# Performance work log

Measured on AMD Instinct MI355X. Metric: run time of the kernel, lower is better.

The kernel has to match this reference:

```python
import jax, jax.numpy as jnp
import numpy as np

DIM = 1024
H = 16
HD = DIM // H
EPS = 1e-5


def setup_inputs() -> dict:
    key = jax.random.key(0)
    ks = jax.random.split(key, 12)
    B, S = 4, 2048
    s = 0.02
    return {
        "q": jax.random.normal(ks[0], (B, S, DIM), jnp.float32),
        "k": jax.random.normal(ks[1], (B, S, DIM), jnp.float32),
        "v": jax.random.normal(ks[2], (B, S, DIM), jnp.float32),
        "Wq": jax.random.normal(ks[3], (DIM, DIM), jnp.float32) * s,
        "bq": jnp.zeros((DIM,), jnp.float32),
        "Wk": jax.random.normal(ks[4], (DIM, DIM), jnp.float32) * s,
        "bk": jnp.zeros((DIM,), jnp.float32),
        "Wv": jax.random.normal(ks[5], (DIM, DIM), jnp.float32) * s,
        "bv": jnp.zeros((DIM,), jnp.float32),
        "Wo": jax.random.normal(ks[6], (DIM, DIM), jnp.float32) * s,
        "bo": jnp.zeros((DIM,), jnp.float32),
        "gamma": jnp.ones((DIM,), jnp.float32),
        "beta": jnp.zeros((DIM,), jnp.float32),
    }


def reference(q, k, v, Wq, bq, Wk, bk, Wv, bv, Wo, bo, gamma, beta):
    B, S, _ = q.shape
    scale = HD ** -0.5
    # projections -> [B, H, S, HD]
    def proj(x, W, b):
        return (x @ W.T + b).reshape(B, -1, H, HD).transpose(0, 2, 1, 3)
    qh = proj(q, Wq, bq)
    kh = proj(k, Wk, bk)
    vh = proj(v, Wv, bv)
    scores = jnp.einsum("bhsd,bhtd->bhst", qh, kh) * scale  # [B,H,S,S]
    attn = jax.nn.softmax(scores, axis=-1)  # dropout is identity in eval
    out = jnp.einsum("bhst,bhtd->bhsd", attn, vh)
    out = out.transpose(0, 2, 1, 3).reshape(B, S, DIM)
    out = out @ Wo.T + bo
    # LayerNorm
    mu = out.mean(-1, keepdims=True)
    var = out.var(-1, keepdims=True)
    return (out - mu) * jax.lax.rsqrt(var + EPS) * gamma + beta
```

## Files before the change

kernel.cpp:

```cpp
#include <hip/hip_runtime.h>

typedef unsigned short u16;
typedef __attribute__((ext_vector_type(8))) short bf16x8;
typedef __attribute__((ext_vector_type(4))) float f32x4;
typedef __attribute__((ext_vector_type(16))) float f32x16;
typedef __attribute__((ext_vector_type(4))) unsigned short u16x4;
typedef __attribute__((ext_vector_type(4))) unsigned int u32x4;
typedef __attribute__((ext_vector_type(2))) unsigned int u32x2;

#define DIM 1024
#define NH 16
#define HD 64
#define BATCH 4
#define SEQ 2048
#define MROWS (BATCH * SEQ)

__device__ __forceinline__ u16 f2bf(float f) {
  unsigned u = __builtin_bit_cast(unsigned, f);
  return (u16)((u + 0x7fffu + ((u >> 16) & 1u)) >> 16);
}

__device__ __forceinline__ void gload16(const u16* g, u16* l) {
  __builtin_amdgcn_global_load_lds(
      (const __attribute__((address_space(1))) void*)g,
      (__attribute__((address_space(3))) void*)l, 16, 0, 0);
}

__device__ __forceinline__ unsigned cvtpk(float lo, float hi) {
  unsigned r;
  asm("v_cvt_pk_bf16_f32 %0, %1, %2" : "=v"(r) : "v"(lo), "v"(hi));
  return r;
}

__device__ __forceinline__ void plswap(unsigned& a, unsigned& b) {
  asm("v_permlane32_swap_b32 %0, %1" : "+v"(a), "+v"(b));
}

__global__ __launch_bounds__(256) void cvtw_kernel(const float* __restrict__ Wq,
                                                   const float* __restrict__ Wk,
                                                   const float* __restrict__ Wv,
                                                   const float* __restrict__ Wo,
                                                   u16* __restrict__ dst,
                                                   float scale) {
  int i = blockIdx.x * blockDim.x + threadIdx.x;
  int seg = i >> 18;
  int off = i & ((1 << 18) - 1);
  const float* src = (seg == 0) ? Wq : (seg == 1) ? Wk : (seg == 2) ? Wv : Wo;
  float mul = (seg == 0) ? scale : 1.f;
  f32x4 v = ((const f32x4*)src)[off];
  u16x4 o;
  o[0] = f2bf(v[0] * mul);
  o[1] = f2bf(v[1] * mul);
  o[2] = f2bf(v[2] * mul);
  o[3] = f2bf(v[3] * mul);
  ((u16x4*)dst)[i] = o;
}

enum { EPI_QK = 0, EPI_VT = 1, EPI_F32 = 2 };

#define BM 128
#define BN 128
#define BK 64

template <int EPI, bool AF32, bool BF32>
__global__ __launch_bounds__(256) void gemm_nt(const void* __restrict__ Ap,
                                               const void* __restrict__ Bp,
                                               void* __restrict__ C,
                                               const float* __restrict__ bias,
                                               float bscale, int Kdim) {
  __shared__ __attribute__((aligned(16))) u16 Alds[BM * BK];
  __shared__ __attribute__((aligned(16))) u16 Blds[BN * BK];

  const int tid = threadIdx.x;
  const int w = tid >> 6, l = tid & 63;
  const int wr = w >> 1, wc = w & 1;
  const int row0 = blockIdx.y * BM;
  const int col0 = blockIdx.x * BN;
  const int lr = l >> 3;
  const int sp = l & 7;

  f32x4 acc[4][4];
#pragma unroll
  for (int i = 0; i < 4; i++)
#pragma unroll
    for (int j = 0; j < 4; j++) {
      f32x4 z = {0.f, 0.f, 0.f, 0.f};
      acc[i][j] = z;
    }

  for (int k0 = 0; k0 < Kdim; k0 += BK) {
    __syncthreads();
#pragma unroll
    for (int q = 0; q < 4; q++) {
      int chunk = w * 4 + q;
      int r = chunk * 8 + lr;
      int sl = sp ^ (r & 7);
      if constexpr (AF32) {
        const float* s = (const float*)Ap + (size_t)(row0 + r) * Kdim + k0 + sp * 8;
        f32x4 v0 = *(const f32x4*)s;
        f32x4 v1 = *(const f32x4*)(s + 4);
        u32x4 pk;
        pk[0] = cvtpk(v0[0], v0[1]);
        pk[1] = cvtpk(v0[2], v0[3]);
        pk[2] = cvtpk(v1[0], v1[1]);
        pk[3] = cvtpk(v1[2], v1[3]);
        *(u32x4*)&Alds[r * 64 + sl * 8] = pk;
      } else {
        gload16((const u16*)Ap + (size_t)(row0 + r) * Kdim + k0 + sl * 8,
                &Alds[chunk * 512]);
      }
      if constexpr (BF32) {
        const float* s = (const float*)Bp + (size_t)(col0 + r) * Kdim + k0 + sp * 8;
        f32x4 v0 = *(const f32x4*)s;
        f32x4 v1 = *(const f32x4*)(s + 4);
        u32x4 pk;
        pk[0] = cvtpk(v0[0], v0[1]);
        pk[1] = cvtpk(v0[2], v0[3]);
        pk[2] = cvtpk(v1[0], v1[1]);
        pk[3] = cvtpk(v1[2], v1[3]);
        *(u32x4*)&Blds[r * 64 + sl * 8] = pk;
      } else {
        gload16((const u16*)Bp + (size_t)(col0 + r) * Kdim + k0 + sl * 8,
                &Blds[chunk * 512]);
      }
    }
    __syncthreads();

#pragma unroll
    for (int t = 0; t < 2; t++) {
      int slot = (t * 4 + (l >> 4)) ^ (l & 7);
      bf16x8 af[4], bf[4];
#pragma unroll
      for (int i = 0; i < 4; i++) {
        int arow = wr * 64 + i * 16 + (l & 15);
        af[i] = *(const bf16x8*)&Alds[arow * 64 + slot * 8];
        int brow = wc * 64 + i * 16 + (l & 15);
        bf[i] = *(const bf16x8*)&Blds[brow * 64 + slot * 8];
      }
      __builtin_amdgcn_s_setprio(1);
#pragma unroll
      for (int i = 0; i < 4; i++)
#pragma unroll
        for (int j = 0; j < 4; j++)
          acc[i][j] = __builtin_amdgcn_mfma_f32_16x16x32_bf16(af[i], bf[j],
                                                              acc[i][j], 0, 0, 0);
      __builtin_amdgcn_s_setprio(0);
    }
  }

#pragma unroll
  for (int i = 0; i < 4; i++) {
#pragma unroll
    for (int j = 0; j < 4; j++) {
#pragma unroll
      for (int q = 0; q < 4; q++) {
        int m = row0 + wr * 64 + i * 16 + (l >> 4) * 4 + q;
        int n = col0 + wc * 64 + j * 16 + (l & 15);
        float v = acc[i][j][q];
        if (EPI == EPI_QK) {
          v += bias[n] * bscale;
          int b_ = m >> 11, s_ = m & (SEQ - 1), h_ = n >> 6, hd_ = n & 63;
          ((u16*)C)[(((size_t)(b_ * NH + h_) * SEQ + s_) << 6) + hd_] = f2bf(v);
        } else if (EPI == EPI_VT) {
          v += bias[m];
          int b_ = n >> 11, s_ = n & (SEQ - 1);
          ((u16*)C)[((size_t)(b_ * NH + (m >> 6)) * HD + (m & 63)) * SEQ + s_] =
              f2bf(v);
        } else {
          v += bias[n];
          ((float*)C)[(size_t)m * DIM + n] = v;
        }
      }
    }
  }
}

__global__ __launch_bounds__(256, 2) void attn_kernel(const u16* __restrict__ Qh,
                                                      const u16* __restrict__ Kh,
                                                      const u16* __restrict__ Vt,
                                                      u16* __restrict__ AO) {
  __shared__ __attribute__((aligned(16))) u16 Klds[3][64 * 64];
  __shared__ __attribute__((aligned(16))) u16 Vlds[3][64 * 64];

  const int tid = threadIdx.x;
  const int w = tid >> 6, l = tid & 63;
  const int l31 = l & 31, hi = l >> 5;
  const int p = blockIdx.x;
  const int bh = (p & 7) + 8 * (p >> 6);
  const int qt = (p >> 3) & 7;
  const int b_ = bh >> 4, h_ = bh & 15;
  const int lr = l >> 3, sp = l & 7;

  const int qrowA = qt * 256 + w * 64 + l31;
  const int qrowB = qrowA + 32;
  const u16* qpA = Qh + ((size_t)bh * SEQ + qrowA) * HD + hi * 8;
  const u16* qpB = Qh + ((size_t)bh * SEQ + qrowB) * HD + hi * 8;
  bf16x8 qfA[4], qfB[4];
#pragma unroll
  for (int ks = 0; ks < 4; ks++) {
    qfA[ks] = *(const bf16x8*)(qpA + ks * 16);
    qfB[ks] = *(const bf16x8*)(qpB + ks * 16);
  }

  f32x16 oA0, oA1, oB0, oB1;
#pragma unroll
  for (int r = 0; r < 16; r++) {
    oA0[r] = 0.f;
    oA1[r] = 0.f;
    oB0[r] = 0.f;
    oB1[r] = 0.f;
  }
  float lrunA = 0.f, lrunB = 0.f;

  const int chunk = w * 2;
  const int r0 = chunk * 8 + lr, r1 = r0 + 8;
  const int sl0 = sp ^ (lr & 7);
  const size_t kbase = (size_t)bh * SEQ * HD;
  const size_t vbase = (size_t)bh * HD * SEQ;

#define ISSUE(kt, buf)                                                        \
  do {                                                                        \
    gload16(Kh + kbase + ((kt) * 64 + r0) * HD + sl0 * 8,                     \
            &Klds[buf][chunk * 512]);                                         \
    gload16(Vt + vbase + (size_t)r0 * SEQ + (kt) * 64 + sl0 * 8,              \
            &Vlds[buf][chunk * 512]);                                         \
    gload16(Kh + kbase + ((kt) * 64 + r1) * HD + sl0 * 8,                     \
            &Klds[buf][chunk * 512 + 512]);                                   \
    gload16(Vt + vbase + (size_t)r1 * SEQ + (kt) * 64 + sl0 * 8,              \
            &Vlds[buf][chunk * 512 + 512]);                                   \
  } while (0)

  ISSUE(0, 0);

  int cur = 0;
  for (int kt = 0; kt < SEQ / 64; kt++) {
    const int nxt = (cur == 2) ? 0 : cur + 1;
    if (kt < SEQ / 64 - 1) {
      ISSUE(kt + 1, nxt);
      asm volatile("s_waitcnt vmcnt(4)" ::: "memory");
    } else {
      asm volatile("s_waitcnt vmcnt(0)" ::: "memory");
    }
    __builtin_amdgcn_s_barrier();
    __builtin_amdgcn_sched_barrier(0);

    const u16* Kc = Klds[cur];
    const u16* Vc = Vlds[cur];

    f32x16 sA0, sA1, sB0, sB1;
#pragma unroll
    for (int r = 0; r < 16; r++) {
      sA0[r] = 0.f;
      sA1[r] = 0.f;
      sB0[r] = 0.f;
      sB1[r] = 0.f;
    }
    __builtin_amdgcn_s_setprio(1);
#pragma unroll
    for (int ks = 0; ks < 4; ks++) {
      int slot = ((ks * 2 + hi) ^ (l & 7)) * 8;
      bf16x8 kf0 = *(const bf16x8*)&Kc[l31 * 64 + slot];
      bf16x8 kf1 = *(const bf16x8*)&Kc[(32 + l31) * 64 + slot];
      sA0 = __builtin_amdgcn_mfma_f32_32x32x16_bf16(kf0, qfA[ks], sA0, 0, 0, 0);
      sA1 = __builtin_amdgcn_mfma_f32_32x32x16_bf16(kf1, qfA[ks], sA1, 0, 0, 0);
      sB0 = __builtin_amdgcn_mfma_f32_32x32x16_bf16(kf0, qfB[ks], sB0, 0, 0, 0);
      sB1 = __builtin_amdgcn_mfma_f32_32x32x16_bf16(kf1, qfB[ks], sB1, 0, 0, 0);
    }
    __builtin_amdgcn_s_setprio(0);

#pragma unroll
    for (int r = 0; r < 16; r++) {
      sA0[r] = __builtin_amdgcn_exp2f(sA0[r]);
      sA1[r] = __builtin_amdgcn_exp2f(sA1[r]);
      sB0[r] = __builtin_amdgcn_exp2f(sB0[r]);
      sB1[r] = __builtin_amdgcn_exp2f(sB1[r]);
    }
    float ta[16], tb[16];
#pragma unroll
    for (int r = 0; r < 8; r++) {
      ta[r] = sA0[2 * r] + sA0[2 * r + 1];
      ta[8 + r] = sA1[2 * r] + sA1[2 * r + 1];
      tb[r] = sB0[2 * r] + sB0[2 * r + 1];
      tb[8 + r] = sB1[2 * r] + sB1[2 * r + 1];
    }
#pragma unroll
    for (int s2 = 8; s2 > 0; s2 >>= 1)
#pragma unroll
      for (int r = 0; r < 8; r++)
        if (r < s2) {
          ta[r] += ta[r + s2];
          tb[r] += tb[r + s2];
        }
    float psA = ta[0];
    float psB = tb[0];
    psA += __shfl_xor(psA, 32);
    psB += __shfl_xor(psB, 32);
    lrunA += psA;
    lrunB += psB;

    unsigned cwA[2][4][2], cwB[2][4][2];
#pragma unroll
    for (int g = 0; g < 4; g++) {
      cwA[0][g][0] = cvtpk(sA0[4 * g], sA0[4 * g + 1]);
      cwA[0][g][1] = cvtpk(sA0[4 * g + 2], sA0[4 * g + 3]);
      cwA[1][g][0] = cvtpk(sA1[4 * g], sA1[4 * g + 1]);
      cwA[1][g][1] = cvtpk(sA1[4 * g + 2], sA1[4 * g + 3]);
      cwB[0][g][0] = cvtpk(sB0[4 * g], sB0[4 * g + 1]);
      cwB[0][g][1] = cvtpk(sB0[4 * g + 2], sB0[4 * g + 3]);
      cwB[1][g][0] = cvtpk(sB1[4 * g], sB1[4 * g + 1]);
      cwB[1][g][1] = cvtpk(sB1[4 * g + 2], sB1[4 * g + 3]);
    }
    bf16x8 paA[4], paB[4];
#pragma unroll
    for (int ks = 0; ks < 4; ks++) {
      int t = ks >> 1, c = ks & 1;
      {
        unsigned a0 = cwA[t][2 * c][0], b0 = cwA[t][2 * c + 1][0];
        unsigned a1 = cwA[t][2 * c][1], b1 = cwA[t][2 * c + 1][1];
        plswap(a0, b0);
        plswap(a1, b1);
        u32x4 pw;
        pw[0] = a0;
        pw[1] = a1;
        pw[2] = b0;
        pw[3] = b1;
        paA[ks] = __builtin_bit_cast(bf16x8, pw);
      }
      {
        unsigned a0 = cwB[t][2 * c][0], b0 = cwB[t][2 * c + 1][0];
        unsigned a1 = cwB[t][2 * c][1], b1 = cwB[t][2 * c + 1][1];
        plswap(a0, b0);
        plswap(a1, b1);
        u32x4 pw;
        pw[0] = a0;
        pw[1] = a1;
        pw[2] = b0;
        pw[3] = b1;
        paB[ks] = __builtin_bit_cast(bf16x8, pw);
      }
    }

    __builtin_amdgcn_s_setprio(1);
#pragma unroll
    for (int ks = 0; ks < 4; ks++) {
      int slot = ((ks * 2 + hi) ^ (l & 7)) * 8;
      bf16x8 vf0 = *(const bf16x8*)&Vc[l31 * 64 + slot];
      bf16x8 vf1 = *(const bf16x8*)&Vc[(32 + l31) * 64 + slot];
      oA0 = __builtin_amdgcn_mfma_f32_32x32x16_bf16(vf0, paA[ks], oA0, 0, 0, 0);
      oA1 = __builtin_amdgcn_mfma_f32_32x32x16_bf16(vf1, paA[ks], oA1, 0, 0, 0);
      oB0 = __builtin_amdgcn_mfma_f32_32x32x16_bf16(vf0, paB[ks], oB0, 0, 0, 0);
      oB1 = __builtin_amdgcn_mfma_f32_32x32x16_bf16(vf1, paB[ks], oB1, 0, 0, 0);
    }
    __builtin_amdgcn_s_setprio(0);

    cur = nxt;
  }

  float rinvA = 1.f / lrunA;
  float rinvB = 1.f / lrunB;
  u16* orowA = AO + ((size_t)b_ * SEQ + qrowA) * DIM + h_ * HD;
  u16* orowB = AO + ((size_t)b_ * SEQ + qrowB) * DIM + h_ * HD;
#pragma unroll
  for (int g = 0; g < 4; g++) {
    u32x2 s0, s1;
    s0[0] = cvtpk(oA0[4 * g] * rinvA, oA0[4 * g + 1] * rinvA);
    s0[1] = cvtpk(oA0[4 * g + 2] * rinvA, oA0[4 * g + 3] * rinvA);
    s1[0] = cvtpk(oA1[4 * g] * rinvA, oA1[4 * g + 1] * rinvA);
    s1[1] = cvtpk(oA1[4 * g + 2] * rinvA, oA1[4 * g + 3] * rinvA);
    *(u32x2*)(orowA + 8 * g + 4 * hi) = s0;
    *(u32x2*)(orowA + 32 + 8 * g + 4 * hi) = s1;
    s0[0] = cvtpk(oB0[4 * g] * rinvB, oB0[4 * g + 1] * rinvB);
    s0[1] = cvtpk(oB0[4 * g + 2] * rinvB, oB0[4 * g + 3] * rinvB);
    s1[0] = cvtpk(oB1[4 * g] * rinvB, oB1[4 * g + 1] * rinvB);
    s1[1] = cvtpk(oB1[4 * g + 2] * rinvB, oB1[4 * g + 3] * rinvB);
    *(u32x2*)(orowB + 8 * g + 4 * hi) = s0;
    *(u32x2*)(orowB + 32 + 8 * g + 4 * hi) = s1;
  }
}

__global__ __launch_bounds__(256) void ln_kernel(const float* __restrict__ X,
                                                 const float* __restrict__ gamma,
                                                 const float* __restrict__ beta,
                                                 float* __restrict__ out) {
  __shared__ float red[8];
  const int row = blockIdx.x;
  const int tid = threadIdx.x;
  const float* xr = X + (size_t)row * DIM;
  f32x4 v = ((const f32x4*)xr)[tid];
  float s = v[0] + v[1] + v[2] + v[3];
  float ss = v[0] * v[0] + v[1] * v[1] + v[2] * v[2] + v[3] * v[3];
#pragma unroll
  for (int mm = 1; mm <= 32; mm <<= 1) {
    s += __shfl_xor(s, mm);
    ss += __shfl_xor(ss, mm);
  }
  const int w = tid >> 6, l = tid & 63;
  if (l == 0) {
    red[w * 2] = s;
    red[w * 2 + 1] = ss;
  }
  __syncthreads();
  s = red[0] + red[2] + red[4] + red[6];
  ss = red[1] + red[3] + red[5] + red[7];
  float mu = s * (1.f / DIM);
  float var = ss * (1.f / DIM) - mu * mu;
  float rstd = rsqrtf(var + 1e-5f);
  f32x4 g = ((const f32x4*)gamma)[tid];
  f32x4 bt = ((const f32x4*)beta)[tid];
  f32x4 o;
#pragma unroll
  for (int j = 0; j < 4; j++) o[j] = (v[j] - mu) * rstd * g[j] + bt[j];
  ((f32x4*)(out + (size_t)row * DIM))[tid] = o;
}

extern "C" void kernel_launch(void* const* d_in, const int* in_sizes, int n_in,
                              void* d_out, int out_size, void* d_ws,
                              size_t ws_size, hipStream_t stream) {
  (void)in_sizes; (void)n_in; (void)out_size; (void)ws_size;
  const float* q = (const float*)d_in[0];
  const float* k = (const float*)d_in[1];
  const float* v = (const float*)d_in[2];
  const float* Wq = (const float*)d_in[3];
  const float* bq = (const float*)d_in[4];
  const float* Wk = (const float*)d_in[5];
  const float* bk = (const float*)d_in[6];
  const float* Wv = (const float*)d_in[7];
  const float* bv = (const float*)d_in[8];
  const float* Wo = (const float*)d_in[9];
  const float* bo = (const float*)d_in[10];
  const float* gamma = (const float*)d_in[11];
  const float* beta = (const float*)d_in[12];

  char* ws = (char*)d_ws;
  const size_t MiB = 1 << 20;
  u16* Wb = (u16*)(ws + 0 * MiB);
  u16* Wq_b = Wb;
  u16* Wk_b = (u16*)(ws + 2 * MiB);
  u16* Wv_b = (u16*)(ws + 4 * MiB);
  u16* Wo_b = (u16*)(ws + 6 * MiB);
  u16* Qh = (u16*)(ws + 8 * MiB);
  u16* Kh = (u16*)(ws + 24 * MiB);
  u16* Vt = (u16*)(ws + 40 * MiB);
  u16* AO = (u16*)(ws + 56 * MiB);

  const float scale = 0.125f * 1.44269504088896f;

  cvtw_kernel<<<4096, 256, 0, stream>>>(Wq, Wk, Wv, Wo, Wb, scale);

  dim3 blk(256);
  gemm_nt<EPI_QK, true, false><<<dim3(DIM / BN, MROWS / BM), blk, 0, stream>>>(
      q, Wq_b, Qh, bq, scale, DIM);
  gemm_nt<EPI_QK, true, false><<<dim3(DIM / BN, MROWS / BM), blk, 0, stream>>>(
      k, Wk_b, Kh, bk, 1.f, DIM);
  gemm_nt<EPI_VT, false, true><<<dim3(MROWS / BN, DIM / BM), blk, 0, stream>>>(
      Wv_b, v, Vt, bv, 1.f, DIM);

  attn_kernel<<<512, 256, 0, stream>>>(Qh, Kh, Vt, AO);

  gemm_nt<EPI_F32, false, false><<<dim3(DIM / BN, MROWS / BM), blk, 0, stream>>>(
      AO, Wo_b, (float*)d_out, bo, 1.f, DIM);

  ln_kernel<<<MROWS, 256, 0, stream>>>((const float*)d_out, gamma, beta,
                                       (float*)d_out);
}
```

Baseline: 238.6 us.

## Double-buffer LDS tiles in GEMM to overlap next-tile loads with MFMA

```diff
diff --git a/kernel.cpp b/kernel.cpp
--- a/kernel.cpp
+++ b/kernel.cpp
@@ -68,8 +68,8 @@
                                                void* __restrict__ C,
                                                const float* __restrict__ bias,
                                                float bscale, int Kdim) {
-  __shared__ __attribute__((aligned(16))) u16 Alds[BM * BK];
-  __shared__ __attribute__((aligned(16))) u16 Blds[BN * BK];
+  __shared__ __attribute__((aligned(16))) u16 Alds[2][BM * BK];
+  __shared__ __attribute__((aligned(16))) u16 Blds[2][BN * BK];
 
   const int tid = threadIdx.x;
   const int w = tid >> 6, l = tid & 63;
@@ -78,6 +78,7 @@
   const int col0 = blockIdx.x * BN;
   const int lr = l >> 3;
   const int sp = l & 7;
+  const int sl = sp ^ lr;
 
   f32x4 acc[4][4];
 #pragma unroll
@@ -88,44 +89,73 @@
       acc[i][j] = z;
     }
 
-  for (int k0 = 0; k0 < Kdim; k0 += BK) {
-    __syncthreads();
+  f32x4 stA[4][2], stB[4][2];
+
+  auto stage_issue = [&](int k0, int buf) {
 #pragma unroll
     for (int q = 0; q < 4; q++) {
       int chunk = w * 4 + q;
       int r = chunk * 8 + lr;
-      int sl = sp ^ (r & 7);
       if constexpr (AF32) {
-        const float* s = (const float*)Ap + (size_t)(row0 + r) * Kdim + k0 + sp * 8;
-        f32x4 v0 = *(const f32x4*)s;
-        f32x4 v1 = *(const f32x4*)(s + 4);
-        u32x4 pk;
-        pk[0] = cvtpk(v0[0], v0[1]);
-        pk[1] = cvtpk(v0[2], v0[3]);
-        pk[2] = cvtpk(v1[0], v1[1]);
-        pk[3] = cvtpk(v1[2], v1[3]);
-        *(u32x4*)&Alds[r * 64 + sl * 8] = pk;
+        const float* s =
+            (const float*)Ap + (size_t)(row0 + r) * Kdim + k0 + sp * 8;
+        stA[q][0] = *(const f32x4*)s;
+        stA[q][1] = *(const f32x4*)(s + 4);
       } else {
         gload16((const u16*)Ap + (size_t)(row0 + r) * Kdim + k0 + sl * 8,
-                &Alds[chunk * 512]);
+                &Alds[buf][chunk * 512]);
       }
       if constexpr (BF32) {
-        const float* s = (const float*)Bp + (size_t)(col0 + r) * Kdim + k0 + sp * 8;
-        f32x4 v0 = *(const f32x4*)s;
-        f32x4 v1 = *(const f32x4*)(s + 4);
-        u32x4 pk;
-        pk[0] = cvtpk(v0[0], v0[1]);
-        pk[1] = cvtpk(v0[2], v0[3]);
-        pk[2] = cvtpk(v1[0], v1[1]);
-        pk[3] = cvtpk(v1[2], v1[3]);
-        *(u32x4*)&Blds[r * 64 + sl * 8] = pk;
+        const float* s =
+            (const float*)Bp + (size_t)(col0 + r) * Kdim + k0 + sp * 8;
+        stB[q][0] = *(const f32x4*)s;
+        stB[q][1] = *(const f32x4*)(s + 4);
       } else {
         gload16((const u16*)Bp + (size_t)(col0 + r) * Kdim + k0 + sl * 8,
-                &Blds[chunk * 512]);
-      }
-    }
-    __syncthreads();
-
+                &Blds[buf][chunk * 512]);
+      }
+    }
+  };
+
+  auto stage_write = [&](int buf) {
+    if constexpr (AF32) {
+#pragma unroll
+      for (int q = 0; q < 4; q++) {
+        int r = (w * 4 + q) * 8 + lr;
+        u32x4 pk;
+        pk[0] = cvtpk(stA[q][0][0], stA[q][0][1]);
+        pk[1] = cvtpk(stA[q][0][2], stA[q][0][3]);
+        pk[2] = cvtpk(stA[q][1][0], stA[q][1][1]);
+        pk[3] = cvtpk(stA[q][1][2], stA[q][1][3]);
+        *(u32x4*)&Alds[buf][r * 64 + sl * 8] = pk;
+      }
+    }
+    if constexpr (BF32) {
+#pragma unroll
+      for (int q = 0; q < 4; q++) {
+        int r = (w * 4 + q) * 8 + lr;
+        u32x4 pk;
+        pk[0] = cvtpk(stB[q][0][0], stB[q][0][1]);
+        pk[1] = cvtpk(stB[q][0][2], stB[q][0][3]);
+        pk[2] = cvtpk(stB[q][1][0], stB[q][1][1]);
+        pk[3] = cvtpk(stB[q][1][2], stB[q][1][3]);
+        *(u32x4*)&Blds[buf][r * 64 + sl * 8] = pk;
+      }
+    }
+  };
+
+  stage_issue(0, 0);
+  asm volatile("s_waitcnt vmcnt(0)" ::: "memory");
+  stage_write(0);
+  __syncthreads();
+
+  const int NT = Kdim / BK;
+  int cur = 0;
+  for (int kt = 0; kt < NT; kt++) {
+    if (kt < NT - 1) stage_issue((kt + 1) * BK, cur ^ 1);
+
+    const u16* Ab = Alds[cur];
+    const u16* Bb = Blds[cur];
 #pragma unroll
     for (int t = 0; t < 2; t++) {
       int slot = (t * 4 + (l >> 4)) ^ (l & 7);
@@ -133,9 +163,9 @@
 #pragma unroll
       for (int i = 0; i < 4; i++) {
         int arow = wr * 64 + i * 16 + (l & 15);
-        af[i] = *(const bf16x8*)&Alds[arow * 64 + slot * 8];
+        af[i] = *(const bf16x8*)&Ab[arow * 64 + slot * 8];
         int brow = wc * 64 + i * 16 + (l & 15);
-        bf[i] = *(const bf16x8*)&Blds[brow * 64 + slot * 8];
+        bf[i] = *(const bf16x8*)&Bb[brow * 64 + slot * 8];
       }
       __builtin_amdgcn_s_setprio(1);
 #pragma unroll
@@ -145,6 +175,13 @@
           acc[i][j] = __builtin_amdgcn_mfma_f32_16x16x32_bf16(af[i], bf[j],
                                                               acc[i][j], 0, 0, 0);
       __builtin_amdgcn_s_setprio(0);
+    }
+
+    if (kt < NT - 1) {
+      asm volatile("s_waitcnt vmcnt(0)" ::: "memory");
+      stage_write(cur ^ 1);
+      __syncthreads();
+      cur ^= 1;
     }
   }
 
```

After: 235.0 us. About the same (-1.5%).
